# Performance work log

Hardware: AMD Instinct MI355X
Metric: run time of the kernel (lower is better)

## Reference

```python
import jax, jax.numpy as jnp
import numpy as np

B, N, TOPK = 64, 1024, 32
C1, DQ, DH, DO, DMLP = 92, 256, 512, 256, 1024
BN_EPS = 1e-5


def setup_inputs() -> dict:
    key = jax.random.key(0)
    ks = jax.random.split(key, 12)
    d_in = DQ + C1 + 4  # 352: query_embed + probs + bbox
    return {
        "probs": jax.random.normal(ks[0], (B, N, C1), jnp.float32),
        "bbox_coords": jax.random.uniform(ks[1], (B, N, 4), jnp.float32),
        "query_emb": jax.random.normal(ks[2], (N, DQ), jnp.float32),
        "node_emb": jax.random.normal(ks[3], (N, DQ), jnp.float32),
        "mlp_w1": jax.random.normal(ks[4], (d_in, DMLP), jnp.float32) * 0.02,
        "mlp_b1": jnp.zeros((DMLP,), jnp.float32),
        "mlp_w2": jax.random.normal(ks[5], (DMLP, N), jnp.float32) * 0.02,
        "mlp_b2": jnp.zeros((N,), jnp.float32),
        "conv1_w": jax.random.normal(ks[6], (DQ, DH), jnp.float32) * (DQ ** -0.5),
        "conv1_b": jnp.zeros((DH,), jnp.float32),
        "conv2_w": jax.random.normal(ks[7], (DH, DO), jnp.float32) * (DH ** -0.5),
        "conv2_b": jnp.zeros((DO,), jnp.float32),
        "bn_gamma": jnp.ones((DH,), jnp.float32),
        "bn_beta": jnp.zeros((DH,), jnp.float32),
    }


def reference(probs, bbox_coords, query_emb, node_emb, mlp_w1, mlp_b1,
              mlp_w2, mlp_b2, conv1_w, conv1_b, conv2_w, conv2_b,
              bn_gamma, bn_beta):
    b = probs.shape[0]
    # edge-weight MLP (2 layers, relu after first) -> dense adjacency (B,N,N)
    x = jnp.concatenate([jnp.broadcast_to(query_emb[None], (b, N, DQ)), probs, bbox_coords], axis=-1)
    adj = jax.nn.relu(x @ mlp_w1 + mlp_b1) @ mlp_w2 + mlp_b2
    vals, idx = jax.lax.top_k(adj, TOPK)          # (B,N,K) values sorted desc
    cols = idx.reshape(b, -1)                      # (B, N*K) targets
    w = vals.reshape(b, -1)                        # (B, N*K) edge weights
    loop = jnp.arange(N)
    row = jnp.repeat(loop, TOPK)                   # (N*K,) sources, shared
    rows_all = jnp.concatenate([row, loop])        # self-loops appended (fill=1)

    def gcn(xw, bias, c, ww):
        # GCNConv: sym-normalized gather-scale-scatter over edges + self loops
        cols2 = jnp.concatenate([c, loop])
        w2 = jnp.concatenate([ww, jnp.ones((N,), xw.dtype)])
        deg = jax.ops.segment_sum(w2, cols2, num_segments=N)
        dinv = deg ** -0.5
        dinv = jnp.where(jnp.isinf(dinv), 0.0, dinv)
        norm = dinv[rows_all] * w2 * dinv[cols2]
        return jax.ops.segment_sum(norm[:, None] * xw[rows_all], cols2, num_segments=N) + bias

    xw1 = node_emb @ conv1_w                       # shared across batch

    def per_batch(c, ww):
        h = gcn(xw1, conv1_b, c, ww)               # (N, DH)
        mu = h.mean(0)
        var = h.var(0)                             # biased var, as torch BN
        h = (h - mu) / jnp.sqrt(var + BN_EPS) * bn_gamma + bn_beta
        h = jax.nn.relu(h)
        return gcn(h @ conv2_w, conv2_b, c, ww)    # (N, DO)

    out = jax.vmap(per_batch)(cols, w)             # (B, N, DO)
    return out[:, None]                            # (B, 1, N, DO) matches torch stack of unsqueezed outs
```

## Files before the change

kernel.cpp:

```cpp
#include <hip/hip_runtime.h>
#include <stdint.h>

typedef float f32x4 __attribute__((ext_vector_type(4)));
typedef _Float16 h16x8 __attribute__((ext_vector_type(8)));
typedef _Float16 h16;
typedef unsigned short u16;


__global__ void k_split_t(const float* __restrict__ in, h16* __restrict__ out,
                          int Cn, int Ck, int ostride, int doSplit) {
  __shared__ float t[32][33];
  int n0 = blockIdx.x * 32, k0 = blockIdx.y * 32;
  int tx = threadIdx.x, ty = threadIdx.y;
#pragma unroll
  for (int i = 0; i < 4; ++i)
    t[ty + i * 8][tx] = in[(size_t)(k0 + ty + i * 8) * Cn + n0 + tx];
  __syncthreads();
#pragma unroll
  for (int i = 0; i < 4; ++i) {
    int n = n0 + ty + i * 8, k = k0 + tx;
    float v = t[tx][ty + i * 8];
    h16 h = (h16)v;
    size_t base = (size_t)n * ostride + k;
    out[base] = h;
    if (doSplit) {
      out[base + Ck] = h;
      out[base + 2 * Ck] = (h16)(v - (float)h);
    }
  }
}

__global__ void k_xcat(const float* __restrict__ qe, const float* __restrict__ probs,
                       const float* __restrict__ bbox, h16* __restrict__ x, int r0, int n) {
  int i = blockIdx.x * 256 + threadIdx.x;
  if (i >= n) return;
  int rl = i / 352, k = i - rl * 352;
  int R = r0 + rl;
  int nn = R & 1023;
  float v;
  if (k < 256)      v = qe[nn * 256 + k];
  else if (k < 348) v = probs[(size_t)R * 92 + (k - 256)];
  else              v = bbox[(size_t)R * 4 + (k - 348)];
  h16 h = (h16)v;
  h16 l = (h16)(v - (float)h);
  size_t base = (size_t)rl * 704;
  x[base + k] = h; x[base + 352 + k] = l;
}

__global__ void k_xw1(const float* __restrict__ ne, const float* __restrict__ c1w,
                      float* __restrict__ xw1f) {
  int r = blockIdx.x >> 1;
  int d = (blockIdx.x & 1) * 256 + threadIdx.x;
  float s = 0.0f;
  for (int k = 0; k < 256; ++k) s += ne[r * 256 + k] * c1w[k * 512 + d];
  xw1f[r * 512 + d] = s;
}


template<int MODE>
__global__ __launch_bounds__(512, 2)
void k_gemm8(const h16* __restrict__ A, const h16* __restrict__ B, void* __restrict__ Cptr,
             const float* __restrict__ bias, const float* __restrict__ rscale,
             int M, int N, int K, int AK) {
  __shared__ __align__(16) char lds[131072];
  const int tid = threadIdx.x;
  const int lane = tid & 63, wid = tid >> 6;
  const int wr = wid >> 2, wc = wid & 3;

  const int gx = N >> 8;
  const int nwg = gridDim.x, wg = blockIdx.x;
  const int q8 = nwg >> 3, r8 = nwg & 7, xcd = wg & 7, lo = wg >> 3;
  const int swz = (xcd < r8 ? xcd * (q8 + 1) : r8 * (q8 + 1) + (xcd - r8) * q8) + lo;
  const int bx = swz % gx, by = swz / gx;

  const int nt = K >> 6;
  const int srow = tid >> 3, s8 = tid & 7;

  char* ldsA = (char*)lds;
  char* ldsB = (char*)lds + 65536;

  auto stage = [&](const h16* __restrict__ Mat, int rowStride, int tileRowBase,
                   char* ldsBase, int buf, int half, int kbase) {
#pragma unroll
    for (int j = 0; j < 2; ++j) {
      int rl = half * 128 + srow + j * 64;
      int gcol = kbase + ((s8 ^ (rl & 7)) << 3);
      const char* src = (const char*)(Mat + (size_t)(tileRowBase + rl) * rowStride + gcol);
      char* dst = ldsBase + buf * 32768 + half * 16384 + j * 8192 + tid * 16;
      __builtin_amdgcn_global_load_lds((const __attribute__((address_space(1))) void*)src,
                                       (__attribute__((address_space(3))) void*)dst, 16, 0, 0);
    }
  };

  f32x4 acc[8][4] = {};
  h16x8 bfr[4][2];

  auto rdA = [&](int buf, int mf, int ks) -> h16x8 {
    int row = wr * 128 + mf * 16 + (lane & 15);
    int cb = ((ks << 6) + ((lane >> 4) << 4)) ^ ((row & 7) << 4);
    return *(const h16x8*)(ldsA + buf * 32768 + row * 128 + cb);
  };
  auto rdB = [&](int buf, int nf, int ks) -> h16x8 {
    int row = wc * 64 + nf * 16 + (lane & 15);
    int cb = ((ks << 6) + ((lane >> 4) << 4)) ^ ((row & 7) << 4);
    return *(const h16x8*)(ldsB + buf * 32768 + row * 128 + cb);
  };

#define BARRIER() do { asm volatile("" ::: "memory"); \
  __builtin_amdgcn_s_barrier(); asm volatile("" ::: "memory"); } while (0)

#define MFMA16(q, af)                                                          \
  __builtin_amdgcn_s_setprio(1);                                               \
  _Pragma("unroll") for (int m2 = 0; m2 < 2; ++m2)                             \
  _Pragma("unroll") for (int nf = 0; nf < 4; ++nf)                             \
  _Pragma("unroll") for (int ks = 0; ks < 2; ++ks)                             \
    acc[(q) * 2 + m2][nf] = __builtin_amdgcn_mfma_f32_16x16x32_f16(            \
        af[m2][ks], bfr[nf][ks], acc[(q) * 2 + m2][nf], 0, 0, 0);              \
  __builtin_amdgcn_s_setprio(0);

  const int aRow = by * 256, bRow = bx * 256;

  stage(A, AK, aRow, ldsA, 0, 0, 0);
  stage(A, AK, aRow, ldsA, 0, 1, 0);
  stage(B, K, bRow, ldsB, 0, 0, 0);
  stage(B, K, bRow, ldsB, 0, 1, 0);
  stage(B, K, bRow, ldsB, 1, 0, 64);
  stage(B, K, bRow, ldsB, 1, 1, 64);
  asm volatile("s_waitcnt vmcnt(4)" ::: "memory");
  BARRIER();

  for (int T = 0; T < nt; ++T) {
    const int p = T & 1;
    const int tkA = (T + 1) << 6;
    const int aA = (tkA < AK) ? tkA : tkA - AK;
    const int tkB = (T + 2) << 6;
    const bool sA = (T + 1) < nt, sB = (T + 2) < nt;

    {
#pragma unroll
      for (int nf = 0; nf < 4; ++nf)
#pragma unroll
        for (int ks = 0; ks < 2; ++ks) bfr[nf][ks] = rdB(p, nf, ks);
      h16x8 af[2][2];
#pragma unroll
      for (int m2 = 0; m2 < 2; ++m2)
#pragma unroll
        for (int ks = 0; ks < 2; ++ks) af[m2][ks] = rdA(p, m2, ks);
      if (sA) stage(A, AK, aRow, ldsA, p ^ 1, 0, aA);
      BARRIER();
      MFMA16(0, af)
      BARRIER();
    }
    {
      h16x8 af[2][2];
#pragma unroll
      for (int m2 = 0; m2 < 2; ++m2)
#pragma unroll
        for (int ks = 0; ks < 2; ++ks) af[m2][ks] = rdA(p, 2 + m2, ks);
      if (sA) stage(A, AK, aRow, ldsA, p ^ 1, 1, aA);
      BARRIER();
      MFMA16(1, af)
      BARRIER();
    }
    {
      h16x8 af[2][2];
#pragma unroll
      for (int m2 = 0; m2 < 2; ++m2)
#pragma unroll
        for (int ks = 0; ks < 2; ++ks) af[m2][ks] = rdA(p, 4 + m2, ks);
      if (sB) stage(B, K, bRow, ldsB, p, 0, tkB);
      BARRIER();
      MFMA16(2, af)
      BARRIER();
    }
    {
      h16x8 af[2][2];
#pragma unroll
      for (int m2 = 0; m2 < 2; ++m2)
#pragma unroll
        for (int ks = 0; ks < 2; ++ks) af[m2][ks] = rdA(p, 6 + m2, ks);
      if (sB) stage(B, K, bRow, ldsB, p, 1, tkB);
      BARRIER();
      MFMA16(3, af)
      if (sB) { asm volatile("s_waitcnt vmcnt(4)" ::: "memory"); }
      else    { asm volatile("s_waitcnt vmcnt(0)" ::: "memory"); }
      BARRIER();
    }
  }

  const int tM = by * 256 + wr * 128, tN = bx * 256 + wc * 64;
#pragma unroll
  for (int mf = 0; mf < 8; ++mf) {
#pragma unroll
    for (int nf = 0; nf < 4; ++nf) {
      int c = tN + nf * 16 + (lane & 15);
      float bvl = bias[c];
#pragma unroll
      for (int i = 0; i < 4; ++i) {
        int r = tM + mf * 16 + (lane >> 4) * 4 + i;
        float v = acc[mf][nf][i];
        if (MODE == 4) v = v * rscale[r] + bvl;
        else v += bvl;
        if (MODE == 2) {
          ((float*)Cptr)[(size_t)r * N + c] = v;
        } else if (MODE == 4) {
          ((h16*)Cptr)[(size_t)r * N + c] = (h16)v;
        } else {
          v = fmaxf(v, 0.0f);
          h16 h = (h16)v;
          h16 l = (h16)(v - (float)h);
          size_t o = (size_t)r * (2 * N) + c;
          ((h16*)Cptr)[o] = h;
          ((h16*)Cptr)[o + N] = l;
        }
      }
    }
  }
#undef BARRIER
#undef MFMA16
}


template<int MODE, int RELU>
__global__ __launch_bounds__(256)
void k_gemm(const h16* __restrict__ A, const h16* __restrict__ B, void* __restrict__ Cptr,
            const float* __restrict__ bias, const float* __restrict__ rscale,
            int M, int N, int K, int AK, int gx,
            long long sA, long long sB, long long sC) {
  __shared__ __align__(16) h16 As[128 * 32];
  __shared__ __align__(16) h16 Bs[128 * 32];
  const int tid = threadIdx.x;
  const int wid = tid >> 6, lane = tid & 63;
  const int wr = wid >> 1, wc = wid & 1;
  const int bz = blockIdx.y;

  const int nwg = gridDim.x, wg = blockIdx.x;
  const int q = nwg >> 3, r8 = nwg & 7, xcd = wg & 7, lo = wg >> 3;
  const int swz = (xcd < r8 ? xcd * (q + 1) : r8 * (q + 1) + (xcd - r8) * q) + lo;
  const int bx = swz % gx, by = swz / gx;

  const char* gA = (const char*)(A + (size_t)bz * sA + (size_t)by * 128 * AK +
                                 (size_t)(tid >> 2) * AK) + (tid & 3) * 16;
  const char* gB = (const char*)(B + (size_t)bz * sB + (size_t)bx * 128 * K +
                                 (size_t)(tid >> 2) * K) + (tid & 3) * 16;
  char* lAs = (char*)As + wid * 1024;
  char* lBs = (char*)Bs + wid * 1024;
  const long long rowStepA = (long long)64 * AK * 2;
  const long long rowStepB = (long long)64 * K * 2;

  f32x4 acc[4][4] = {};
  const int aoff = (wr * 64 + (lane & 15)) * 32 + (lane >> 4) * 8;
  const int boff = (wc * 64 + (lane & 15)) * 32 + (lane >> 4) * 8;

  for (int kt = 0; kt < K; kt += 32) {
    const int akt = (kt < AK) ? kt : kt - AK;
    __syncthreads();
#pragma unroll
    for (int j = 0; j < 2; ++j) {
      __builtin_amdgcn_global_load_lds(
          (const __attribute__((address_space(1))) void*)(gA + j * rowStepA + (size_t)akt * 2),
          (__attribute__((address_space(3))) void*)(lAs + j * 4096), 16, 0, 0);
      __builtin_amdgcn_global_load_lds(
          (const __attribute__((address_space(1))) void*)(gB + j * rowStepB + (size_t)kt * 2),
          (__attribute__((address_space(3))) void*)(lBs + j * 4096), 16, 0, 0);
    }
    asm volatile("s_waitcnt vmcnt(0)" ::: "memory");
    __syncthreads();

    h16x8 af[4], bv[4];
#pragma unroll
    for (int m = 0; m < 4; ++m) af[m] = *(const h16x8*)(As + aoff + m * 512);
#pragma unroll
    for (int n = 0; n < 4; ++n) bv[n] = *(const h16x8*)(Bs + boff + n * 512);
#pragma unroll
    for (int m = 0; m < 4; ++m)
#pragma unroll
      for (int n = 0; n < 4; ++n)
        acc[m][n] = __builtin_amdgcn_mfma_f32_16x16x32_f16(af[m], bv[n], acc[m][n], 0, 0, 0);
  }

  const int tM = by * 128 + wr * 64, tN = bx * 128 + wc * 64;
#pragma unroll
  for (int m = 0; m < 4; ++m) {
#pragma unroll
    for (int n = 0; n < 4; ++n) {
      int c = tN + n * 16 + (lane & 15);
      float bvl = bias ? bias[c] : 0.0f;
#pragma unroll
      for (int i = 0; i < 4; ++i) {
        int r = tM + m * 16 + (lane >> 4) * 4 + i;
        float v = acc[m][n][i];
        if (rscale) v *= rscale[bz * 1024 + r];
        v += bvl;
        if (RELU) v = fmaxf(v, 0.0f);
        if (MODE == 1) {
          size_t o = ((size_t)(r >> 10) * N + c) * 1024 + (r & 1023);
          ((h16*)Cptr)[o] = (h16)v;
        } else if (MODE == 2) {
          size_t o = (size_t)bz * sC + (size_t)r * N + c;
          ((float*)Cptr)[o] = v;
        }
      }
    }
  }
}


__global__ void k_topk(const float* __restrict__ adj, float* __restrict__ vals,
                       u16* __restrict__ idxo, int r0) {
  __shared__ unsigned binsAll[4][256];
  const int wv = threadIdx.x >> 6, lane = threadIdx.x & 63;
  unsigned* bins = binsAll[wv];
  const int rl = blockIdx.x * 4 + wv;

  float v[16]; unsigned key[16];
  const float4* rp = (const float4*)(adj + (size_t)rl * 1024 + lane * 16);
#pragma unroll
  for (int q = 0; q < 4; ++q) {
    float4 t = rp[q];
    v[4 * q] = t.x; v[4 * q + 1] = t.y; v[4 * q + 2] = t.z; v[4 * q + 3] = t.w;
  }
#pragma unroll
  for (int j = 0; j < 16; ++j) {
    unsigned b = __float_as_uint(v[j]);
    key[j] = b ^ (unsigned)(((int)b >> 31) | (int)0x80000000);
  }

  unsigned pfx = 0; int need = 32;
#pragma unroll
  for (int lvl = 0; lvl < 4; ++lvl) {
    const int shift = 24 - lvl * 8;
    bins[lane] = 0; bins[lane + 64] = 0; bins[lane + 128] = 0; bins[lane + 192] = 0;
    __syncthreads();
#pragma unroll
    for (int j = 0; j < 16; ++j) {
      bool cand = (lvl == 0) || ((key[j] >> (shift + 8)) == pfx);
      if (cand) atomicAdd(&bins[(key[j] >> shift) & 255u], 1u);
    }
    __syncthreads();
    int c0 = (int)bins[lane * 4 + 0], c1 = (int)bins[lane * 4 + 1],
        c2 = (int)bins[lane * 4 + 2], c3 = (int)bins[lane * 4 + 3];
    int s = c0 + c1 + c2 + c3;
    int inc = s;
#pragma unroll
    for (int off = 1; off < 64; off <<= 1) {
      int t = __shfl_down(inc, off);
      if (lane + off < 64) inc += t;
    }
    int gt3 = inc - s;
    int gt2 = gt3 + c3, gt1 = gt2 + c2, gt0 = gt1 + c1;
    int tloc = -1, gtsel = 0;
    if (gt3 < need && gt3 + c3 >= need) { tloc = lane * 4 + 3; gtsel = gt3; }
    if (gt2 < need && gt2 + c2 >= need) { tloc = lane * 4 + 2; gtsel = gt2; }
    if (gt1 < need && gt1 + c1 >= need) { tloc = lane * 4 + 1; gtsel = gt1; }
    if (gt0 < need && gt0 + c0 >= need) { tloc = lane * 4 + 0; gtsel = gt0; }
    unsigned long long bal = __ballot(tloc >= 0);
    int src = __ffsll(bal) - 1;
    int t   = __shfl(tloc, src);
    int gtv = __shfl(gtsel, src);
    pfx = (pfx << 8) | (unsigned)t;
    need -= gtv;
    __syncthreads();
  }

  unsigned sureMask = 0, tieMask = 0;
#pragma unroll
  for (int j = 0; j < 16; ++j) {
    if (key[j] > pfx) sureMask |= (1u << j);
    else if (key[j] == pfx) tieMask |= (1u << j);
  }
  int cs = __popc(sureMask), ct = __popc(tieMask);
  int incS = cs, incT = ct;
#pragma unroll
  for (int off = 1; off < 64; off <<= 1) {
    int a = __shfl_up(incS, off);
    int b2 = __shfl_up(incT, off);
    if (lane >= off) { incS += a; incT += b2; }
  }
  int baseS = incS - cs, baseT = incT - ct;
  int totalS = __shfl(incS, 63);
  size_t obase = ((size_t)(r0 + rl)) * 32;
  int o = baseS;
#pragma unroll
  for (int j = 0; j < 16; ++j)
    if (sureMask & (1u << j)) {
      vals[obase + o] = v[j];
      idxo[obase + o] = (u16)(lane * 16 + j);
      ++o;
    }
  int o2 = totalS + baseT;
#pragma unroll
  for (int j = 0; j < 16; ++j)
    if (tieMask & (1u << j)) {
      if (o2 < 32) { vals[obase + o2] = v[j]; idxo[obase + o2] = (u16)(lane * 16 + j); }
      ++o2;
    }
}


__global__ void k_deg_init(float* deg) {
  int i = blockIdx.x * 256 + threadIdx.x;
  if (i < 65536) deg[i] = 1.0f;
}

__global__ void k_deg_acc(const float* __restrict__ vals, const u16* __restrict__ idxo,
                          float* __restrict__ deg) {
  int e = blockIdx.x * 256 + threadIdx.x;
  int b = e >> 15;
  atomicAdd(&deg[b * 1024 + (int)idxo[e]], vals[e]);
}

__global__ void k_dinv(const float* __restrict__ deg, float* __restrict__ dinv) {
  int i = blockIdx.x * 256 + threadIdx.x;
  if (i >= 65536) return;
  float d = deg[i];
  float r = 1.0f / sqrtf(d);
  if (isinf(r)) r = 0.0f;
  dinv[i] = r;
}

__global__ void k_self(const float* __restrict__ dinv, h16* __restrict__ Wd, int g) {
  int i = blockIdx.x * 256 + threadIdx.x;
  if (i >= 16384) return;
  int bl = i >> 10, c = i & 1023;
  Wd[((size_t)bl << 20) + (size_t)c * 1024 + c] = (h16)dinv[g * 16384 + i];
}

__global__ void k_edge(const float* __restrict__ vals, const u16* __restrict__ idxo,
                       const float* __restrict__ dinv, h16* __restrict__ Wd, int g) {
  int e = blockIdx.x * 256 + threadIdx.x;
  if (e >= 524288) return;
  int bl = e >> 15;
  int r = (e >> 5) & 1023;
  size_t E = (size_t)g * 524288 + e;
  int c = (int)idxo[E];
  float w = vals[E] * dinv[g * 16384 + (bl << 10) + r];
  size_t o = ((size_t)bl << 20) + (size_t)c * 1024 + r;
  Wd[o] = (h16)((float)Wd[o] + w);
}


__global__ void k_bnpart(const h16* __restrict__ h1, float2* __restrict__ part) {
  int b = blockIdx.x, seg = blockIdx.y, d = threadIdx.x;
  size_t base = ((size_t)(b * 1024 + seg * 128)) * 512 + d;
  float s = 0.0f, ss = 0.0f;
  for (int n = 0; n < 128; ++n) {
    float h = (float)h1[base + (size_t)n * 512];
    s += h; ss += h * h;
  }
  part[(size_t)(b * 8 + seg) * 512 + d] = make_float2(s, ss);
}

__global__ void k_bnfin(const float2* __restrict__ part, float* __restrict__ mu,
                        float* __restrict__ rstd) {
  int i = blockIdx.x * 256 + threadIdx.x;
  if (i >= 8192) return;
  int b = i >> 9, d = i & 511;
  float s = 0.0f, ss = 0.0f;
  for (int seg = 0; seg < 8; ++seg) {
    float2 t = part[(size_t)(b * 8 + seg) * 512 + d];
    s += t.x; ss += t.y;
  }
  float m = s * (1.0f / 1024.0f);
  float var = ss * (1.0f / 1024.0f) - m * m;
  mu[b * 512 + d] = m;
  rstd[b * 512 + d] = 1.0f / sqrtf(var + 1e-5f);
}

__global__ void k_bnapply(h16* __restrict__ h1, const float* __restrict__ mu,
                          const float* __restrict__ rstd, const float* __restrict__ gamma,
                          const float* __restrict__ beta) {
  int i = blockIdx.x * 256 + threadIdx.x;
  if (i >= 16 * 1024 * 512) return;
  int d = i & 511;
  int b = i >> 19;
  float y = ((float)h1[i] - mu[b * 512 + d]) * rstd[b * 512 + d] * gamma[d] + beta[d];
  h1[i] = (h16)fmaxf(y, 0.0f);
}


extern "C" void kernel_launch(void* const* d_in, const int* in_sizes, int n_in,
                              void* d_out, int out_size, void* d_ws, size_t ws_size,
                              hipStream_t stream) {
  const float* probs = (const float*)d_in[0];
  const float* bbox  = (const float*)d_in[1];
  const float* qe    = (const float*)d_in[2];
  const float* ne    = (const float*)d_in[3];
  const float* w1    = (const float*)d_in[4];
  const float* b1    = (const float*)d_in[5];
  const float* w2    = (const float*)d_in[6];
  const float* b2    = (const float*)d_in[7];
  const float* c1w   = (const float*)d_in[8];
  const float* c1b   = (const float*)d_in[9];
  const float* c2w   = (const float*)d_in[10];
  const float* c2b   = (const float*)d_in[11];
  const float* gamma = (const float*)d_in[12];
  const float* beta  = (const float*)d_in[13];

  if (ws_size < 82444288ULL) return;
  const bool big = ws_size >= 115998720ULL;
  const int CH = big ? 16384 : 8192;
  const int NCH = 65536 / CH;

  char* p = (char*)d_ws;
  h16* W1cat = (h16*)p; p += (size_t)1024 * 1088 * 2;
  h16* W2cat = (h16*)p; p += (size_t)1024 * 3072 * 2;
  h16* c2wt  = (h16*)p; p += (size_t)256 * 512 * 2;
  float* xw1f = (float*)p; p += (size_t)1024 * 512 * 4;
  h16*  xw1t = (h16*)p;  p += (size_t)512 * 1024 * 2;
  float* vals = (float*)p; p += (size_t)2097152 * 4;
  u16*   idxo = (u16*)p;   p += (size_t)2097152 * 2;
  float* deg  = (float*)p; p += (size_t)65536 * 4;
  float* dinv = (float*)p; p += (size_t)65536 * 4;
  float* mu   = (float*)p; p += (size_t)64 * 512 * 4;
  float* rstd = (float*)p; p += (size_t)64 * 512 * 4;
  float2* bnp = (float2*)p; p += (size_t)16 * 8 * 512 * 8;
  char* R1 = p;
  h16* Xcat  = (h16*)R1;
  h16* Hcat2 = (h16*)(R1 + (size_t)CH * 704 * 2);
  h16* Wd   = (h16*)R1;
  h16* h1   = (h16*)(R1 + 33554432);
  h16* xw2t = (h16*)(R1 + 50331648);
  float* adjf = (float*)d_out;

  hipMemsetAsync(W1cat, 0, (size_t)1024 * 1088 * 2, stream);
  k_split_t<<<dim3(32, 11), dim3(32, 8), 0, stream>>>(w1, W1cat, 1024, 352, 1088, 1);
  k_split_t<<<dim3(32, 32), dim3(32, 8), 0, stream>>>(w2, W2cat, 1024, 1024, 3072, 1);
  k_split_t<<<dim3(8, 16), dim3(32, 8), 0, stream>>>(c2w, c2wt, 256, 512, 512, 0);
  k_xw1<<<2048, 256, 0, stream>>>(ne, c1w, xw1f);
  k_split_t<<<dim3(16, 32), dim3(32, 8), 0, stream>>>(xw1f, xw1t, 512, 1024, 1024, 0);

  for (int c = 0; c < NCH; ++c) {
    int r0 = c * CH;
    k_xcat<<<(CH * 352) / 256, 256, 0, stream>>>(qe, probs, bbox, Xcat, r0, CH * 352);
    k_gemm8<3><<<(CH / 256) * 4, 512, 0, stream>>>(Xcat, W1cat, Hcat2, b1, nullptr,
                                                   CH, 1024, 1088, 704);
    k_gemm8<2><<<(CH / 256) * 4, 512, 0, stream>>>(Hcat2, W2cat, adjf, b2, nullptr,
                                                   CH, 1024, 3072, 2048);
    k_topk<<<CH / 4, 256, 0, stream>>>(adjf, vals, idxo, r0);
  }

  k_deg_init<<<256, 256, 0, stream>>>(deg);
  k_deg_acc<<<8192, 256, 0, stream>>>(vals, idxo, deg);
  k_dinv<<<256, 256, 0, stream>>>(deg, dinv);

  for (int g = 0; g < 4; ++g) {
    const float* dg = dinv + g * 16384;
    hipMemsetAsync(Wd, 0, (size_t)33554432, stream);
    k_self<<<64, 256, 0, stream>>>(dinv, Wd, g);
    k_edge<<<2048, 256, 0, stream>>>(vals, idxo, dinv, Wd, g);
    k_gemm8<4><<<128, 512, 0, stream>>>(Wd, xw1t, h1, c1b, dg, 16384, 512, 1024, 1024);
    k_bnpart<<<dim3(16, 8), 512, 0, stream>>>(h1, bnp);
    k_bnfin<<<32, 256, 0, stream>>>(bnp, mu, rstd);
    k_bnapply<<<32768, 256, 0, stream>>>(h1, mu, rstd, gamma, beta);
    k_gemm<1, 0><<<dim3(256, 1), 256, 0, stream>>>(h1, c2wt, xw2t, nullptr, nullptr,
                                                   16384, 256, 512, 512, 2, 0, 0, 0);
    k_gemm<2, 0><<<dim3(16, 16), 256, 0, stream>>>(Wd, xw2t,
                                                   (float*)d_out + (size_t)g * 16 * 262144,
                                                   c2b, dg, 1024, 256, 1024, 1024, 2,
                                                   1048576LL, 262144LL, 262144LL);
  }
}
```

Baseline: 1.411 ms.

## Fuse BN stats into GEMM epilogue, degree into topk, sparse Wd wipe

The BN partial-sum kernel is removed. The GEMM epilogue (new MODE 5) accumulates per-column sum and sum of squares and atomically adds them into a zeroed buffer. Degree accumulation moves into the top-k kernel via atomics, and the per-group 32MB memset of the dense adjacency is replaced by a kernel that zeroes only the entries written by the previous group. Top-k swaps block-wide barriers for per-wave LDS waits, since each wave owns its own bins. This cuts memory traffic and launches, in exchange for atomic contention and a dependence on exactly undoing the previous group's writes.

After: 1.454 ms. 3.1% more time.

```diff
diff --git a/kernel.cpp b/kernel.cpp
--- a/kernel.cpp
+++ b/kernel.cpp
@@ -5,6 +5,9 @@
 typedef _Float16 h16x8 __attribute__((ext_vector_type(8)));
 typedef _Float16 h16;
 typedef unsigned short u16;
+
+#define WSYNC() do { asm volatile("s_waitcnt lgkmcnt(0)" ::: "memory"); \
+  __builtin_amdgcn_sched_barrier(0); } while (0)
 
 
 __global__ void k_split_t(const float* __restrict__ in, h16* __restrict__ out,
@@ -61,7 +64,7 @@
 __global__ __launch_bounds__(512, 2)
 void k_gemm8(const h16* __restrict__ A, const h16* __restrict__ B, void* __restrict__ Cptr,
              const float* __restrict__ bias, const float* __restrict__ rscale,
-             int M, int N, int K, int AK) {
+             float2* __restrict__ bnp, int M, int N, int K, int AK) {
   __shared__ __align__(16) char lds[131072];
   const int tid = threadIdx.x;
   const int lane = tid & 63, wid = tid >> 6;
@@ -189,6 +192,7 @@
   }
 
   const int tM = by * 256 + wr * 128, tN = bx * 256 + wc * 64;
+  float sl[4] = {0.f, 0.f, 0.f, 0.f}, ssl[4] = {0.f, 0.f, 0.f, 0.f};
 #pragma unroll
   for (int mf = 0; mf < 8; ++mf) {
 #pragma unroll
@@ -199,12 +203,13 @@
       for (int i = 0; i < 4; ++i) {
         int r = tM + mf * 16 + (lane >> 4) * 4 + i;
         float v = acc[mf][nf][i];
-        if (MODE == 4) v = v * rscale[r] + bvl;
+        if (MODE == 5) v = v * rscale[r] + bvl;
         else v += bvl;
         if (MODE == 2) {
           ((float*)Cptr)[(size_t)r * N + c] = v;
-        } else if (MODE == 4) {
+        } else if (MODE == 5) {
           ((h16*)Cptr)[(size_t)r * N + c] = (h16)v;
+          sl[nf] += v; ssl[nf] += v * v;
         } else {
           v = fmaxf(v, 0.0f);
           h16 h = (h16)v;
@@ -213,6 +218,20 @@
           ((h16*)Cptr)[o] = h;
           ((h16*)Cptr)[o + N] = l;
         }
+      }
+    }
+  }
+  if (MODE == 5) {
+    int b = by >> 2;
+#pragma unroll
+    for (int nf = 0; nf < 4; ++nf) {
+      float s = sl[nf], ss = ssl[nf];
+      s += __shfl_xor(s, 16); ss += __shfl_xor(ss, 16);
+      s += __shfl_xor(s, 32); ss += __shfl_xor(ss, 32);
+      if (lane < 16) {
+        int c = tN + nf * 16 + lane;
+        atomicAdd(&bnp[b * 512 + c].x, s);
+        atomicAdd(&bnp[b * 512 + c].y, ss);
       }
     }
   }
@@ -307,7 +326,7 @@
 
 
 __global__ void k_topk(const float* __restrict__ adj, float* __restrict__ vals,
-                       u16* __restrict__ idxo, int r0) {
+                       u16* __restrict__ idxo, float* __restrict__ deg, int r0) {
   __shared__ unsigned binsAll[4][256];
   const int wv = threadIdx.x >> 6, lane = threadIdx.x & 63;
   unsigned* bins = binsAll[wv];
@@ -331,15 +350,16 @@
   for (int lvl = 0; lvl < 4; ++lvl) {
     const int shift = 24 - lvl * 8;
     bins[lane] = 0; bins[lane + 64] = 0; bins[lane + 128] = 0; bins[lane + 192] = 0;
-    __syncthreads();
+    WSYNC();
 #pragma unroll
     for (int j = 0; j < 16; ++j) {
       bool cand = (lvl == 0) || ((key[j] >> (shift + 8)) == pfx);
       if (cand) atomicAdd(&bins[(key[j] >> shift) & 255u], 1u);
     }
-    __syncthreads();
+    WSYNC();
     int c0 = (int)bins[lane * 4 + 0], c1 = (int)bins[lane * 4 + 1],
         c2 = (int)bins[lane * 4 + 2], c3 = (int)bins[lane * 4 + 3];
+    WSYNC();
     int s = c0 + c1 + c2 + c3;
     int inc = s;
 #pragma unroll
@@ -360,7 +380,6 @@
     int gtv = __shfl(gtsel, src);
     pfx = (pfx << 8) | (unsigned)t;
     need -= gtv;
-    __syncthreads();
   }
 
   unsigned sureMask = 0, tieMask = 0;
@@ -380,19 +399,25 @@
   int baseS = incS - cs, baseT = incT - ct;
   int totalS = __shfl(incS, 63);
   size_t obase = ((size_t)(r0 + rl)) * 32;
+  int degb = ((r0 + rl) >> 10) << 10;
   int o = baseS;
 #pragma unroll
   for (int j = 0; j < 16; ++j)
     if (sureMask & (1u << j)) {
       vals[obase + o] = v[j];
       idxo[obase + o] = (u16)(lane * 16 + j);
+      atomicAdd(&deg[degb + lane * 16 + j], v[j]);
       ++o;
     }
   int o2 = totalS + baseT;
 #pragma unroll
   for (int j = 0; j < 16; ++j)
     if (tieMask & (1u << j)) {
-      if (o2 < 32) { vals[obase + o2] = v[j]; idxo[obase + o2] = (u16)(lane * 16 + j); }
+      if (o2 < 32) {
+        vals[obase + o2] = v[j];
+        idxo[obase + o2] = (u16)(lane * 16 + j);
+        atomicAdd(&deg[degb + lane * 16 + j], v[j]);
+      }
       ++o2;
     }
 }
@@ -401,13 +426,6 @@
 __global__ void k_deg_init(float* deg) {
   int i = blockIdx.x * 256 + threadIdx.x;
   if (i < 65536) deg[i] = 1.0f;
-}
-
-__global__ void k_deg_acc(const float* __restrict__ vals, const u16* __restrict__ idxo,
-                          float* __restrict__ deg) {
-  int e = blockIdx.x * 256 + threadIdx.x;
-  int b = e >> 15;
-  atomicAdd(&deg[b * 1024 + (int)idxo[e]], vals[e]);
 }
 
 __global__ void k_dinv(const float* __restrict__ deg, float* __restrict__ dinv) {
@@ -439,32 +457,31 @@
   Wd[o] = (h16)((float)Wd[o] + w);
 }
 
-
-__global__ void k_bnpart(const h16* __restrict__ h1, float2* __restrict__ part) {
-  int b = blockIdx.x, seg = blockIdx.y, d = threadIdx.x;
-  size_t base = ((size_t)(b * 1024 + seg * 128)) * 512 + d;
-  float s = 0.0f, ss = 0.0f;
-  for (int n = 0; n < 128; ++n) {
-    float h = (float)h1[base + (size_t)n * 512];
-    s += h; ss += h * h;
-  }
-  part[(size_t)(b * 8 + seg) * 512 + d] = make_float2(s, ss);
-}
+__global__ void k_wipe(const u16* __restrict__ idxo, h16* __restrict__ Wd, int g) {
+  int t = blockIdx.x * 256 + threadIdx.x;
+  if (t < 524288) {
+    int bl = t >> 15, r = (t >> 5) & 1023;
+    int c = (int)idxo[(size_t)g * 524288 + t];
+    Wd[((size_t)bl << 20) + (size_t)c * 1024 + r] = (h16)0.0f;
+  } else {
+    int i = t - 524288;
+    if (i < 16384) {
+      int bl = i >> 10, c = i & 1023;
+      Wd[((size_t)bl << 20) + (size_t)c * 1024 + c] = (h16)0.0f;
+    }
+  }
+}
+
 
 __global__ void k_bnfin(const float2* __restrict__ part, float* __restrict__ mu,
                         float* __restrict__ rstd) {
   int i = blockIdx.x * 256 + threadIdx.x;
   if (i >= 8192) return;
-  int b = i >> 9, d = i & 511;
-  float s = 0.0f, ss = 0.0f;
-  for (int seg = 0; seg < 8; ++seg) {
-    float2 t = part[(size_t)(b * 8 + seg) * 512 + d];
-    s += t.x; ss += t.y;
-  }
-  float m = s * (1.0f / 1024.0f);
-  float var = ss * (1.0f / 1024.0f) - m * m;
-  mu[b * 512 + d] = m;
-  rstd[b * 512 + d] = 1.0f / sqrtf(var + 1e-5f);
+  float2 t = part[i];
+  float m = t.x * (1.0f / 1024.0f);
+  float var = t.y * (1.0f / 1024.0f) - m * m;
+  mu[i] = m;
+  rstd[i] = 1.0f / sqrtf(var + 1e-5f);
 }
 
 __global__ void k_bnapply(h16* __restrict__ h1, const float* __restrict__ mu,
@@ -529,28 +546,28 @@
   k_split_t<<<dim3(8, 16), dim3(32, 8), 0, stream>>>(c2w, c2wt, 256, 512, 512, 0);
   k_xw1<<<2048, 256, 0, stream>>>(ne, c1w, xw1f);
   k_split_t<<<dim3(16, 32), dim3(32, 8), 0, stream>>>(xw1f, xw1t, 512, 1024, 1024, 0);
+  k_deg_init<<<256, 256, 0, stream>>>(deg);
 
   for (int c = 0; c < NCH; ++c) {
     int r0 = c * CH;
     k_xcat<<<(CH * 352) / 256, 256, 0, stream>>>(qe, probs, bbox, Xcat, r0, CH * 352);
     k_gemm8<3><<<(CH / 256) * 4, 512, 0, stream>>>(Xcat, W1cat, Hcat2, b1, nullptr,
-                                                   CH, 1024, 1088, 704);
+                                                   nullptr, CH, 1024, 1088, 704);
     k_gemm8<2><<<(CH / 256) * 4, 512, 0, stream>>>(Hcat2, W2cat, adjf, b2, nullptr,
-                                                   CH, 1024, 3072, 2048);
-    k_topk<<<CH / 4, 256, 0, stream>>>(adjf, vals, idxo, r0);
-  }
-
-  k_deg_init<<<256, 256, 0, stream>>>(deg);
-  k_deg_acc<<<8192, 256, 0, stream>>>(vals, idxo, deg);
+                                                   nullptr, CH, 1024, 3072, 2048);
+    k_topk<<<CH / 4, 256, 0, stream>>>(adjf, vals, idxo, deg, r0);
+  }
+
   k_dinv<<<256, 256, 0, stream>>>(deg, dinv);
 
   for (int g = 0; g < 4; ++g) {
     const float* dg = dinv + g * 16384;
-    hipMemsetAsync(Wd, 0, (size_t)33554432, stream);
+    if (g == 0) hipMemsetAsync(Wd, 0, (size_t)33554432, stream);
     k_self<<<64, 256, 0, stream>>>(dinv, Wd, g);
     k_edge<<<2048, 256, 0, stream>>>(vals, idxo, dinv, Wd, g);
-    k_gemm8<4><<<128, 512, 0, stream>>>(Wd, xw1t, h1, c1b, dg, 16384, 512, 1024, 1024);
-    k_bnpart<<<dim3(16, 8), 512, 0, stream>>>(h1, bnp);
+    hipMemsetAsync(bnp, 0, (size_t)16 * 512 * 8, stream);
+    k_gemm8<5><<<128, 512, 0, stream>>>(Wd, xw1t, h1, c1b, dg, bnp,
+                                        16384, 512, 1024, 1024);
     k_bnfin<<<32, 256, 0, stream>>>(bnp, mu, rstd);
     k_bnapply<<<32768, 256, 0, stream>>>(h1, mu, rstd, gamma, beta);
     k_gemm<1, 0><<<dim3(256, 1), 256, 0, stream>>>(h1, c2wt, xw2t, nullptr, nullptr,
@@ -559,5 +576,6 @@
                                                    (float*)d_out + (size_t)g * 16 * 262144,
                                                    c2b, dg, 1024, 256, 1024, 1024, 2,
                                                    1048576LL, 262144LL, 262144LL);
-  }
-}
+    if (g < 3) k_wipe<<<2112, 256, 0, stream>>>(idxo, Wd, g);
+  }
+}
```

## Replace dense GCN adjacency GEMMs with CSR sparse gather aggregation

Applied to the files above, without the earlier changes.

Replaces the dense per-batch normalized adjacency matrix, built via memset and scatter and then multiplied with MFMA GEMMs, with a CSR built by counting sort (count, scan, fill). Two wave-per-node gather kernels then perform the GCN aggregation for both layers. This removes the 32MB memsets and the dense 1024x1024 GEMMs, which mostly multiply zeros given only 32 edges per row. The costs are atomic-based CSR construction, irregular gathers and nondeterministic edge order, and the BN apply step is also vectorized.

Result: slower. 2.760 ms (+95.7%).

```diff
diff --git a/kernel.cpp b/kernel.cpp
--- a/kernel.cpp
+++ b/kernel.cpp
@@ -3,6 +3,7 @@
 
 typedef float f32x4 __attribute__((ext_vector_type(4)));
 typedef _Float16 h16x8 __attribute__((ext_vector_type(8)));
+typedef _Float16 h16x4 __attribute__((ext_vector_type(4)));
 typedef _Float16 h16;
 typedef unsigned short u16;
 
@@ -48,20 +49,19 @@
 }
 
 __global__ void k_xw1(const float* __restrict__ ne, const float* __restrict__ c1w,
-                      float* __restrict__ xw1f) {
+                      h16* __restrict__ xw1h) {
   int r = blockIdx.x >> 1;
   int d = (blockIdx.x & 1) * 256 + threadIdx.x;
   float s = 0.0f;
   for (int k = 0; k < 256; ++k) s += ne[r * 256 + k] * c1w[k * 512 + d];
-  xw1f[r * 512 + d] = s;
+  xw1h[r * 512 + d] = (h16)s;
 }
 
 
 template<int MODE>
 __global__ __launch_bounds__(512, 2)
 void k_gemm8(const h16* __restrict__ A, const h16* __restrict__ B, void* __restrict__ Cptr,
-             const float* __restrict__ bias, const float* __restrict__ rscale,
-             int M, int N, int K, int AK) {
+             const float* __restrict__ bias, int M, int N, int K, int AK) {
   __shared__ __align__(16) char lds[131072];
   const int tid = threadIdx.x;
   const int lane = tid & 63, wid = tid >> 6;
@@ -134,7 +134,7 @@
     const int tkA = (T + 1) << 6;
     const int aA = (tkA < AK) ? tkA : tkA - AK;
     const int tkB = (T + 2) << 6;
-    const bool sA = (T + 1) < nt, sB = (T + 2) < nt;
+    const bool sAn = (T + 1) < nt, sBn = (T + 2) < nt;
 
     {
 #pragma unroll
@@ -146,7 +146,7 @@
       for (int m2 = 0; m2 < 2; ++m2)
 #pragma unroll
         for (int ks = 0; ks < 2; ++ks) af[m2][ks] = rdA(p, m2, ks);
-      if (sA) stage(A, AK, aRow, ldsA, p ^ 1, 0, aA);
+      if (sAn) stage(A, AK, aRow, ldsA, p ^ 1, 0, aA);
       BARRIER();
       MFMA16(0, af)
       BARRIER();
@@ -157,7 +157,7 @@
       for (int m2 = 0; m2 < 2; ++m2)
 #pragma unroll
         for (int ks = 0; ks < 2; ++ks) af[m2][ks] = rdA(p, 2 + m2, ks);
-      if (sA) stage(A, AK, aRow, ldsA, p ^ 1, 1, aA);
+      if (sAn) stage(A, AK, aRow, ldsA, p ^ 1, 1, aA);
       BARRIER();
       MFMA16(1, af)
       BARRIER();
@@ -168,7 +168,7 @@
       for (int m2 = 0; m2 < 2; ++m2)
 #pragma unroll
         for (int ks = 0; ks < 2; ++ks) af[m2][ks] = rdA(p, 4 + m2, ks);
-      if (sB) stage(B, K, bRow, ldsB, p, 0, tkB);
+      if (sBn) stage(B, K, bRow, ldsB, p, 0, tkB);
       BARRIER();
       MFMA16(2, af)
       BARRIER();
@@ -179,11 +179,11 @@
       for (int m2 = 0; m2 < 2; ++m2)
 #pragma unroll
         for (int ks = 0; ks < 2; ++ks) af[m2][ks] = rdA(p, 6 + m2, ks);
-      if (sB) stage(B, K, bRow, ldsB, p, 1, tkB);
+      if (sBn) stage(B, K, bRow, ldsB, p, 1, tkB);
       BARRIER();
       MFMA16(3, af)
-      if (sB) { asm volatile("s_waitcnt vmcnt(4)" ::: "memory"); }
-      else    { asm volatile("s_waitcnt vmcnt(0)" ::: "memory"); }
+      if (sBn) { asm volatile("s_waitcnt vmcnt(4)" ::: "memory"); }
+      else     { asm volatile("s_waitcnt vmcnt(0)" ::: "memory"); }
       BARRIER();
     }
   }
@@ -198,13 +198,9 @@
 #pragma unroll
       for (int i = 0; i < 4; ++i) {
         int r = tM + mf * 16 + (lane >> 4) * 4 + i;
-        float v = acc[mf][nf][i];
-        if (MODE == 4) v = v * rscale[r] + bvl;
-        else v += bvl;
+        float v = acc[mf][nf][i] + bvl;
         if (MODE == 2) {
           ((float*)Cptr)[(size_t)r * N + c] = v;
-        } else if (MODE == 4) {
-          ((h16*)Cptr)[(size_t)r * N + c] = (h16)v;
         } else {
           v = fmaxf(v, 0.0f);
           h16 h = (h16)v;
@@ -221,47 +217,42 @@
 }
 
 
-template<int MODE, int RELU>
+template<int MODE>
 __global__ __launch_bounds__(256)
 void k_gemm(const h16* __restrict__ A, const h16* __restrict__ B, void* __restrict__ Cptr,
-            const float* __restrict__ bias, const float* __restrict__ rscale,
-            int M, int N, int K, int AK, int gx,
-            long long sA, long long sB, long long sC) {
+            int M, int N, int K, int gx) {
   __shared__ __align__(16) h16 As[128 * 32];
   __shared__ __align__(16) h16 Bs[128 * 32];
   const int tid = threadIdx.x;
   const int wid = tid >> 6, lane = tid & 63;
   const int wr = wid >> 1, wc = wid & 1;
-  const int bz = blockIdx.y;
 
   const int nwg = gridDim.x, wg = blockIdx.x;
   const int q = nwg >> 3, r8 = nwg & 7, xcd = wg & 7, lo = wg >> 3;
   const int swz = (xcd < r8 ? xcd * (q + 1) : r8 * (q + 1) + (xcd - r8) * q) + lo;
   const int bx = swz % gx, by = swz / gx;
 
-  const char* gA = (const char*)(A + (size_t)bz * sA + (size_t)by * 128 * AK +
-                                 (size_t)(tid >> 2) * AK) + (tid & 3) * 16;
-  const char* gB = (const char*)(B + (size_t)bz * sB + (size_t)bx * 128 * K +
-                                 (size_t)(tid >> 2) * K) + (tid & 3) * 16;
+  const char* gA = (const char*)(A + (size_t)by * 128 * K + (size_t)(tid >> 2) * K) +
+                   (tid & 3) * 16;
+  const char* gB = (const char*)(B + (size_t)bx * 128 * K + (size_t)(tid >> 2) * K) +
+                   (tid & 3) * 16;
   char* lAs = (char*)As + wid * 1024;
   char* lBs = (char*)Bs + wid * 1024;
-  const long long rowStepA = (long long)64 * AK * 2;
-  const long long rowStepB = (long long)64 * K * 2;
+  const long long rowStep = (long long)64 * K * 2;
 
   f32x4 acc[4][4] = {};
   const int aoff = (wr * 64 + (lane & 15)) * 32 + (lane >> 4) * 8;
   const int boff = (wc * 64 + (lane & 15)) * 32 + (lane >> 4) * 8;
 
   for (int kt = 0; kt < K; kt += 32) {
-    const int akt = (kt < AK) ? kt : kt - AK;
     __syncthreads();
 #pragma unroll
     for (int j = 0; j < 2; ++j) {
       __builtin_amdgcn_global_load_lds(
-          (const __attribute__((address_space(1))) void*)(gA + j * rowStepA + (size_t)akt * 2),
+          (const __attribute__((address_space(1))) void*)(gA + j * rowStep + (size_t)kt * 2),
           (__attribute__((address_space(3))) void*)(lAs + j * 4096), 16, 0, 0);
       __builtin_amdgcn_global_load_lds(
-          (const __attribute__((address_space(1))) void*)(gB + j * rowStepB + (size_t)kt * 2),
+          (const __attribute__((address_space(1))) void*)(gB + j * rowStep + (size_t)kt * 2),
           (__attribute__((address_space(3))) void*)(lBs + j * 4096), 16, 0, 0);
     }
     asm volatile("s_waitcnt vmcnt(0)" ::: "memory");
@@ -285,21 +276,10 @@
 #pragma unroll
     for (int n = 0; n < 4; ++n) {
       int c = tN + n * 16 + (lane & 15);
-      float bvl = bias ? bias[c] : 0.0f;
 #pragma unroll
       for (int i = 0; i < 4; ++i) {
         int r = tM + m * 16 + (lane >> 4) * 4 + i;
-        float v = acc[m][n][i];
-        if (rscale) v *= rscale[bz * 1024 + r];
-        v += bvl;
-        if (RELU) v = fmaxf(v, 0.0f);
-        if (MODE == 1) {
-          size_t o = ((size_t)(r >> 10) * N + c) * 1024 + (r & 1023);
-          ((h16*)Cptr)[o] = (h16)v;
-        } else if (MODE == 2) {
-          size_t o = (size_t)bz * sC + (size_t)r * N + c;
-          ((float*)Cptr)[o] = v;
-        }
+        if (MODE == 4) ((h16*)Cptr)[(size_t)r * N + c] = (h16)acc[m][n][i];
       }
     }
   }
@@ -419,24 +399,118 @@
   dinv[i] = r;
 }
 
-__global__ void k_self(const float* __restrict__ dinv, h16* __restrict__ Wd, int g) {
+
+__global__ void k_cnt(const u16* __restrict__ idxo, unsigned* __restrict__ cnt) {
+  int e = blockIdx.x * 256 + threadIdx.x;
+  atomicAdd(&cnt[((e >> 15) << 10) + (int)idxo[e]], 1u);
+}
+
+__global__ void k_scanA(const unsigned* __restrict__ cnt, unsigned* __restrict__ off,
+                        unsigned* __restrict__ bsum) {
+  __shared__ unsigned s[256];
+  int t = threadIdx.x, base = blockIdx.x * 256;
+  unsigned v = cnt[base + t];
+  s[t] = v; __syncthreads();
+  for (int o = 1; o < 256; o <<= 1) {
+    unsigned u = (t >= o) ? s[t - o] : 0u;
+    __syncthreads(); s[t] += u; __syncthreads();
+  }
+  off[base + t] = s[t] - v;
+  if (t == 255) bsum[blockIdx.x] = s[255];
+}
+
+__global__ void k_scanB(unsigned* __restrict__ bsum) {
+  __shared__ unsigned s[256];
+  int t = threadIdx.x;
+  unsigned v = bsum[t];
+  s[t] = v; __syncthreads();
+  for (int o = 1; o < 256; o <<= 1) {
+    unsigned u = (t >= o) ? s[t - o] : 0u;
+    __syncthreads(); s[t] += u; __syncthreads();
+  }
+  bsum[t] = s[t] - v;
+}
+
+__global__ void k_scanC(unsigned* __restrict__ off, const unsigned* __restrict__ bsum,
+                        unsigned* __restrict__ cur) {
   int i = blockIdx.x * 256 + threadIdx.x;
-  if (i >= 16384) return;
-  int bl = i >> 10, c = i & 1023;
-  Wd[((size_t)bl << 20) + (size_t)c * 1024 + c] = (h16)dinv[g * 16384 + i];
-}
-
-__global__ void k_edge(const float* __restrict__ vals, const u16* __restrict__ idxo,
-                       const float* __restrict__ dinv, h16* __restrict__ Wd, int g) {
+  unsigned o = off[i] + bsum[i >> 8];
+  off[i] = o; cur[i] = o;
+}
+
+__global__ void k_fill(const float* __restrict__ vals, const u16* __restrict__ idxo,
+                       const float* __restrict__ dinv, unsigned* __restrict__ cur,
+                       u16* __restrict__ er, h16* __restrict__ ew) {
   int e = blockIdx.x * 256 + threadIdx.x;
-  if (e >= 524288) return;
-  int bl = e >> 15;
+  int b = e >> 15;
   int r = (e >> 5) & 1023;
-  size_t E = (size_t)g * 524288 + e;
-  int c = (int)idxo[E];
-  float w = vals[E] * dinv[g * 16384 + (bl << 10) + r];
-  size_t o = ((size_t)bl << 20) + (size_t)c * 1024 + r;
-  Wd[o] = (h16)((float)Wd[o] + w);
+  int c = (int)idxo[e];
+  unsigned slot = atomicAdd(&cur[b * 1024 + c], 1u);
+  er[slot] = (u16)r;
+  ew[slot] = (h16)(vals[e] * dinv[b * 1024 + r]);
+}
+
+
+__global__ void k_spmm1(const u16* __restrict__ er, const h16* __restrict__ ew,
+                        const unsigned* __restrict__ cnt, const unsigned* __restrict__ off,
+                        const h16* __restrict__ xw1h, const float* __restrict__ dinv,
+                        const float* __restrict__ c1b, h16* __restrict__ h1, int gb0) {
+  const int wv = threadIdx.x >> 6, lane = threadIdx.x & 63;
+  const int Dl = blockIdx.x * 4 + wv;
+  const int Dg = gb0 * 1024 + Dl;
+  const int c = Dl & 1023;
+  const float dc = dinv[Dg];
+  const int len = (int)cnt[Dg];
+  const unsigned o = off[Dg];
+
+  h16x8 xs = *(const h16x8*)(xw1h + c * 512 + lane * 8);
+  float acc[8];
+#pragma unroll
+  for (int j = 0; j < 8; ++j) acc[j] = dc * (float)xs[j];
+
+  for (int i = 0; i < len; ++i) {
+    int r = (int)er[o + i];
+    float w = (float)ew[o + i];
+    h16x8 xv = *(const h16x8*)(xw1h + r * 512 + lane * 8);
+#pragma unroll
+    for (int j = 0; j < 8; ++j) acc[j] += w * (float)xv[j];
+  }
+
+  h16x8 ov;
+#pragma unroll
+  for (int j = 0; j < 8; ++j) ov[j] = (h16)(dc * acc[j] + c1b[lane * 8 + j]);
+  *(h16x8*)(h1 + (size_t)Dl * 512 + lane * 8) = ov;
+}
+
+__global__ void k_spmm2(const u16* __restrict__ er, const h16* __restrict__ ew,
+                        const unsigned* __restrict__ cnt, const unsigned* __restrict__ off,
+                        const h16* __restrict__ xw2c, const float* __restrict__ dinv,
+                        const float* __restrict__ c2b, float* __restrict__ out, int gb0) {
+  const int wv = threadIdx.x >> 6, lane = threadIdx.x & 63;
+  const int Dl = blockIdx.x * 4 + wv;
+  const int Dg = gb0 * 1024 + Dl;
+  const int c = Dl & 1023;
+  const int bl = Dl >> 10;
+  const float dc = dinv[Dg];
+  const int len = (int)cnt[Dg];
+  const unsigned o = off[Dg];
+
+  h16x4 xs = *(const h16x4*)(xw2c + (size_t)(bl * 1024 + c) * 256 + lane * 4);
+  float acc[4];
+#pragma unroll
+  for (int j = 0; j < 4; ++j) acc[j] = dc * (float)xs[j];
+
+  for (int i = 0; i < len; ++i) {
+    int r = (int)er[o + i];
+    float w = (float)ew[o + i];
+    h16x4 xv = *(const h16x4*)(xw2c + (size_t)(bl * 1024 + r) * 256 + lane * 4);
+#pragma unroll
+    for (int j = 0; j < 4; ++j) acc[j] += w * (float)xv[j];
+  }
+
+#pragma unroll
+  for (int j = 0; j < 4; ++j)
+    out[(size_t)Dg * 256 + lane * 4 + j] = dc * acc[j] + c2b[lane * 4 + j];
 }
 
 
@@ -452,9 +526,9 @@
 }
 
 __global__ void k_bnfin(const float2* __restrict__ part, float* __restrict__ mu,
-                        float* __restrict__ rstd) {
+                        float* __restrict__ rstd, int n) {
   int i = blockIdx.x * 256 + threadIdx.x;
-  if (i >= 8192) return;
+  if (i >= n) return;
   int b = i >> 9, d = i & 511;
   float s = 0.0f, ss = 0.0f;
   for (int seg = 0; seg < 8; ++seg) {
@@ -463,19 +537,27 @@
   }
   float m = s * (1.0f / 1024.0f);
   float var = ss * (1.0f / 1024.0f) - m * m;
-  mu[b * 512 + d] = m;
-  rstd[b * 512 + d] = 1.0f / sqrtf(var + 1e-5f);
+  mu[i] = m;
+  rstd[i] = 1.0f / sqrtf(var + 1e-5f);
 }
 
 __global__ void k_bnapply(h16* __restrict__ h1, const float* __restrict__ mu,
                           const float* __restrict__ rstd, const float* __restrict__ gamma,
-                          const float* __restrict__ beta) {
+                          const float* __restrict__ beta, int n8) {
   int i = blockIdx.x * 256 + threadIdx.x;
-  if (i >= 16 * 1024 * 512) return;
-  int d = i & 511;
-  int b = i >> 19;
-  float y = ((float)h1[i] - mu[b * 512 + d]) * rstd[b * 512 + d] * gamma[d] + beta[d];
-  h1[i] = (h16)fmaxf(y, 0.0f);
+  if (i >= n8) return;
+  int i8 = i * 8;
+  int d0 = i8 & 511;
+  int b = i8 >> 19;
+  h16x8 hv = *(const h16x8*)(h1 + i8);
+  h16x8 ov;
+#pragma unroll
+  for (int j = 0; j < 8; ++j) {
+    int d = d0 + j;
+    float y = ((float)hv[j] - mu[b * 512 + d]) * rstd[b * 512 + d] * gamma[d] + beta[d];
+    ov[j] = (h16)fmaxf(y, 0.0f);
+  }
+  *(h16x8*)(h1 + i8) = ov;
 }
 
 
@@ -501,41 +583,46 @@
   const bool big = ws_size >= 115998720ULL;
   const int CH = big ? 16384 : 8192;
   const int NCH = 65536 / CH;
+  const int CHG = big ? 64 : 32;
+  const int NG = 64 / CHG;
 
   char* p = (char*)d_ws;
   h16* W1cat = (h16*)p; p += (size_t)1024 * 1088 * 2;
   h16* W2cat = (h16*)p; p += (size_t)1024 * 3072 * 2;
   h16* c2wt  = (h16*)p; p += (size_t)256 * 512 * 2;
-  float* xw1f = (float*)p; p += (size_t)1024 * 512 * 4;
-  h16*  xw1t = (h16*)p;  p += (size_t)512 * 1024 * 2;
+  h16* xw1h  = (h16*)p; p += (size_t)1024 * 512 * 2;
   float* vals = (float*)p; p += (size_t)2097152 * 4;
   u16*   idxo = (u16*)p;   p += (size_t)2097152 * 2;
   float* deg  = (float*)p; p += (size_t)65536 * 4;
   float* dinv = (float*)p; p += (size_t)65536 * 4;
   float* mu   = (float*)p; p += (size_t)64 * 512 * 4;
   float* rstd = (float*)p; p += (size_t)64 * 512 * 4;
-  float2* bnp = (float2*)p; p += (size_t)16 * 8 * 512 * 8;
+  float2* bnp = (float2*)p; p += (size_t)64 * 8 * 512 * 8;
   char* R1 = p;
   h16* Xcat  = (h16*)R1;
   h16* Hcat2 = (h16*)(R1 + (size_t)CH * 704 * 2);
-  h16* Wd   = (h16*)R1;
-  h16* h1   = (h16*)(R1 + 33554432);
-  h16* xw2t = (h16*)(R1 + 50331648);
+  unsigned* cnt  = (unsigned*)R1;
+  unsigned* eoff = (unsigned*)(R1 + 262144);
+  unsigned* cur  = (unsigned*)(R1 + 524288);
+  unsigned* bsum = (unsigned*)(R1 + 786432);
+  u16* er = (u16*)(R1 + 790528);
+  h16* ew = (h16*)(R1 + 4984832);
+  h16* h1 = (h16*)(R1 + 9179136);
+  h16* xw2c = (h16*)(R1 + 9179136 + (size_t)CHG * 1048576);
   float* adjf = (float*)d_out;
 
   hipMemsetAsync(W1cat, 0, (size_t)1024 * 1088 * 2, stream);
   k_split_t<<<dim3(32, 11), dim3(32, 8), 0, stream>>>(w1, W1cat, 1024, 352, 1088, 1);
   k_split_t<<<dim3(32, 32), dim3(32, 8), 0, stream>>>(w2, W2cat, 1024, 1024, 3072, 1);
   k_split_t<<<dim3(8, 16), dim3(32, 8), 0, stream>>>(c2w, c2wt, 256, 512, 512, 0);
-  k_xw1<<<2048, 256, 0, stream>>>(ne, c1w, xw1f);
-  k_split_t<<<dim3(16, 32), dim3(32, 8), 0, stream>>>(xw1f, xw1t, 512, 1024, 1024, 0);
+  k_xw1<<<2048, 256, 0, stream>>>(ne, c1w, xw1h);
 
   for (int c = 0; c < NCH; ++c) {
     int r0 = c * CH;
     k_xcat<<<(CH * 352) / 256, 256, 0, stream>>>(qe, probs, bbox, Xcat, r0, CH * 352);
-    k_gemm8<3><<<(CH / 256) * 4, 512, 0, stream>>>(Xcat, W1cat, Hcat2, b1, nullptr,
+    k_gemm8<3><<<(CH / 256) * 4, 512, 0, stream>>>(Xcat, W1cat, Hcat2, b1,
                                                    CH, 1024, 1088, 704);
-    k_gemm8<2><<<(CH / 256) * 4, 512, 0, stream>>>(Hcat2, W2cat, adjf, b2, nullptr,
+    k_gemm8<2><<<(CH / 256) * 4, 512, 0, stream>>>(Hcat2, W2cat, adjf, b2,
                                                    CH, 1024, 3072, 2048);
     k_topk<<<CH / 4, 256, 0, stream>>>(adjf, vals, idxo, r0);
   }
@@ -544,20 +631,24 @@
   k_deg_acc<<<8192, 256, 0, stream>>>(vals, idxo, deg);
   k_dinv<<<256, 256, 0, stream>>>(deg, dinv);
 
-  for (int g = 0; g < 4; ++g) {
-    const float* dg = dinv + g * 16384;
-    hipMemsetAsync(Wd, 0, (size_t)33554432, stream);
-    k_self<<<64, 256, 0, stream>>>(dinv, Wd, g);
-    k_edge<<<2048, 256, 0, stream>>>(vals, idxo, dinv, Wd, g);
-    k_gemm8<4><<<128, 512, 0, stream>>>(Wd, xw1t, h1, c1b, dg, 16384, 512, 1024, 1024);
-    k_bnpart<<<dim3(16, 8), 512, 0, stream>>>(h1, bnp);
-    k_bnfin<<<32, 256, 0, stream>>>(bnp, mu, rstd);
-    k_bnapply<<<32768, 256, 0, stream>>>(h1, mu, rstd, gamma, beta);
-    k_gemm<1, 0><<<dim3(256, 1), 256, 0, stream>>>(h1, c2wt, xw2t, nullptr, nullptr,
-                                                   16384, 256, 512, 512, 2, 0, 0, 0);
-    k_gemm<2, 0><<<dim3(16, 16), 256, 0, stream>>>(Wd, xw2t,
-                                                   (float*)d_out + (size_t)g * 16 * 262144,
-                                                   c2b, dg, 1024, 256, 1024, 1024, 2,
-                                                   1048576LL, 262144LL, 262144LL);
-  }
-}
+  hipMemsetAsync(cnt, 0, 262144, stream);
+  k_cnt<<<8192, 256, 0, stream>>>(idxo, cnt);
+  k_scanA<<<256, 256, 0, stream>>>(cnt, eoff, bsum);
+  k_scanB<<<1, 256, 0, stream>>>(bsum);
+  k_scanC<<<256, 256, 0, stream>>>(eoff, bsum, cur);
+  k_fill<<<8192, 256, 0, stream>>>(vals, idxo, dinv, cur, er, ew);
+
+  for (int g = 0; g < NG; ++g) {
+    int gb0 = g * CHG;
+    k_spmm1<<<CHG * 256, 256, 0, stream>>>(er, ew, cnt, eoff, xw1h, dinv, c1b, h1, gb0);
+    k_bnpart<<<dim3(CHG, 8), 512, 0, stream>>>(h1, bnp);
+    k_bnfin<<<(CHG * 512) / 256, 256, 0, stream>>>(bnp, mu, rstd, CHG * 512);
+    k_bnapply<<<CHG * 256, 256, 0, stream>>>(h1, mu, rstd, gamma, beta, CHG * 65536);
+    for (int sc = 0; sc < CHG / 16; ++sc) {
+      k_gemm<4><<<256, 256, 0, stream>>>(h1 + (size_t)sc * 16 * 1024 * 512, c2wt, xw2c,
+                                         16384, 256, 512, 2);
+      k_spmm2<<<4096, 256, 0, stream>>>(er, ew, cnt, eoff, xw2c, dinv, c2b,
+                                        (float*)d_out, gb0 + sc * 16);
+    }
+  }
+}
```
